# Kernel tuning notes

Hardware: AMD Instinct MI355X
Metric: run time of the kernel (lower is better)

Reference implementation:

```python
import jax, jax.numpy as jnp
import numpy as np

BATCH, SEQLEN, D_MODEL, D_STATE = 2, 2048, 512, 64
DT_MIN, DT_MAX = 1e-4, 1e-3


def setup_inputs() -> dict:
    key = jax.random.key(0)
    k1, k2, k3, k4 = jax.random.split(key, 4)
    u = jax.random.normal(k1, (BATCH, SEQLEN, D_MODEL), dtype=jnp.float32)
    # real parts of the complex params B, C (imag parts never affect the output)
    B_re = (jax.random.normal(k2, (D_STATE,), dtype=jnp.float32) / np.float32(np.sqrt(D_STATE)))
    C_re = (jax.random.normal(k3, (D_STATE,), dtype=jnp.float32) / np.float32(np.sqrt(D_STATE)))
    log_dt = jax.random.uniform(k4, (D_MODEL,), minval=np.log(DT_MIN), maxval=np.log(DT_MAX)).astype(jnp.float32)
    D = jnp.ones((D_MODEL,), dtype=jnp.float32)
    return {"u": u, "B_re": B_re, "C_re": C_re, "log_dt": log_dt, "D": D}


def reference(u, B_re, C_re, log_dt, D):
    # u: [B, L, H]; B_re/C_re: [N]; log_dt/D: [H]
    N = B_re.shape[0]
    # buffer: log_A = -0.5 * log(1 + n/N), n = 1..N  (A = exp(log_A) in (0,1])
    log_A = -0.5 * jnp.log1p(jnp.arange(1, N + 1, dtype=jnp.float32) / N)
    A = jnp.exp(log_A)                       # [N]
    delta = jnp.exp(log_dt)                  # [H]
    A_d = jnp.exp(delta[:, None] * A[None, :])          # [H, N]
    B_d = (A_d - 1.0) * B_re[None, :] * delta[:, None]  # [H, N]

    Bsz, L, H = u.shape
    x0 = jnp.zeros((Bsz, H, N), dtype=u.dtype)

    def step(x, u_t):                        # x: [B,H,N], u_t: [B,H]
        x = A_d * x + B_d * u_t[..., None]
        y_t = jnp.einsum('bhn,n->bh', x, C_re) + D * u_t
        return x, y_t

    _, ys = jax.lax.scan(step, x0, jnp.swapaxes(u, 0, 1))  # ys: [L,B,H]
    return jnp.swapaxes(ys, 0, 1)                          # [B,L,H]
```

## Files before the change

kernel.cpp:

```cpp
#include <hip/hip_runtime.h>
#include <math.h>


#define BATCH   2
#define SEQLEN  2048
#define DMODEL  512
#define DSTATE  64
#define T_CHUNK 32
#define NCHUNK  64

__device__ __forceinline__ float A_cont(int n) {
    return rsqrtf(1.0f + (float)(n + 1) * (1.0f / 64.0f));
}

__global__ __launch_bounds__(256) void k_tables(const float* __restrict__ B_re,
                                                const float* __restrict__ log_dt,
                                                float* __restrict__ AdT,
                                                float* __restrict__ BdT) {
    int tid = blockIdx.x * 256 + threadIdx.x;
    int h = tid & (DMODEL - 1);
    int n = tid >> 9;
    float delta = expf(log_dt[h]);
    float dA = delta * A_cont(n);
    AdT[n * DMODEL + h] = expf(dA);
    BdT[n * DMODEL + h] = expm1f(dA) * B_re[n] * delta;
}

__global__ __launch_bounds__(256) void k_xlocal(const float* __restrict__ u,
                                                const float* __restrict__ AdT,
                                                const float* __restrict__ BdT,
                                                float* __restrict__ xl) {
    int bid = (int)blockIdx.x;
    int wb  = (bid & 7) * 128 + (bid >> 3);
    int tid = wb * 256 + (int)threadIdx.x;
    int h  = tid & (DMODEL - 1);
    int ng = (tid >> 9) & 3;
    int c  = (tid >> 11) & (NCHUNK - 1);
    int b  = tid >> 17;
    int n0 = ng * 16;
    float Ad[16], Bd[16], x[16];
    #pragma unroll
    for (int nn = 0; nn < 16; ++nn) {
        Ad[nn] = AdT[(size_t)(n0 + nn) * DMODEL + h];
        Bd[nn] = BdT[(size_t)(n0 + nn) * DMODEL + h];
        x[nn] = 0.0f;
    }
    const float* up = u + ((size_t)(b * SEQLEN + c * T_CHUNK)) * DMODEL + h;
    #pragma unroll 8
    for (int s = 0; s < T_CHUNK; ++s) {
        float uv = up[(size_t)s * DMODEL];
        #pragma unroll
        for (int nn = 0; nn < 16; ++nn)
            x[nn] = fmaf(Ad[nn], x[nn], Bd[nn] * uv);
    }
    float* xp = xl + ((size_t)((b * NCHUNK + c) * DSTATE + n0)) * DMODEL + h;
    #pragma unroll
    for (int nn = 0; nn < 16; ++nn) xp[(size_t)nn * DMODEL] = x[nn];
}

__global__ __launch_bounds__(256) void k_scan(const float* __restrict__ log_dt,
                                              float* __restrict__ xl) {
    int tid = blockIdx.x * 256 + threadIdx.x;
    int h = tid & (DMODEL - 1);
    int n = (tid >> 9) & (DSTATE - 1);
    int b = tid >> 15;
    float delta = expf(log_dt[h]);
    float ApT = expf(delta * A_cont(n) * (float)T_CHUNK);
    float* base = xl + ((size_t)(b * NCHUNK * DSTATE + n)) * DMODEL + h;
    float v[NCHUNK - 1];
    #pragma unroll
    for (int c = 0; c < NCHUNK - 1; ++c)
        v[c] = base[(size_t)c * DSTATE * DMODEL];
    float s = 0.0f;
    #pragma unroll
    for (int c = 0; c < NCHUNK - 1; ++c) { s = fmaf(ApT, s, v[c]); v[c] = s; }
    #pragma unroll
    for (int c = 0; c < NCHUNK - 1; ++c)
        base[(size_t)c * DSTATE * DMODEL] = v[c];
}

__global__ __launch_bounds__(256) void k_y(const float* __restrict__ u,
                                           const float* __restrict__ AdT,
                                           const float* __restrict__ BdT,
                                           const float* __restrict__ C_re,
                                           const float* __restrict__ Dp,
                                           const float* __restrict__ Sbuf,
                                           float* __restrict__ out) {
    int bid = (int)blockIdx.x;
    int wb  = (bid & 7) * 128 + (bid >> 3);
    int tid = wb * 256 + (int)threadIdx.x;
    int hl = tid & 15;
    int ng = (tid >> 4) & 3;
    int hm = (tid >> 6) & 31;
    int h  = hl | (hm << 4);
    int c  = (tid >> 11) & (NCHUNK - 1);
    int b  = tid >> 17;
    int n0 = ng * 16;

    float Ad[16], Bd[16], Cw[16], x[16];
    #pragma unroll
    for (int nn = 0; nn < 16; ++nn) {
        Ad[nn] = AdT[(size_t)(n0 + nn) * DMODEL + h];
        Bd[nn] = BdT[(size_t)(n0 + nn) * DMODEL + h];
        Cw[nn] = C_re[n0 + nn];
    }
    if (c > 0) {
        const float* sp = Sbuf + ((size_t)((b * NCHUNK + (c - 1)) * DSTATE + n0)) * DMODEL + h;
        #pragma unroll
        for (int nn = 0; nn < 16; ++nn) x[nn] = sp[(size_t)nn * DMODEL];
    } else {
        #pragma unroll
        for (int nn = 0; nn < 16; ++nn) x[nn] = 0.0f;
    }
    float Dv = Dp[h];
    const float* up = u   + ((size_t)(b * SEQLEN + c * T_CHUNK)) * DMODEL + h;
    float*       op = out + ((size_t)(b * SEQLEN + c * T_CHUNK)) * DMODEL + h;
    int store_lane = ((threadIdx.x & 48) == 0);

    #pragma unroll 4
    for (int t = 0; t < T_CHUNK; ++t) {
        float uv = up[(size_t)t * DMODEL];
        #pragma unroll
        for (int nn = 0; nn < 16; ++nn)
            x[nn] = fmaf(Ad[nn], x[nn], Bd[nn] * uv);
        float a0 = 0.0f, a1 = 0.0f, a2 = 0.0f, a3 = 0.0f;
        #pragma unroll
        for (int nn = 0; nn < 16; nn += 4) {
            a0 = fmaf(Cw[nn + 0], x[nn + 0], a0);
            a1 = fmaf(Cw[nn + 1], x[nn + 1], a1);
            a2 = fmaf(Cw[nn + 2], x[nn + 2], a2);
            a3 = fmaf(Cw[nn + 3], x[nn + 3], a3);
        }
        float acc = (a0 + a1) + (a2 + a3);
        acc += __shfl_xor(acc, 16);
        acc += __shfl_xor(acc, 32);
        if (store_lane)
            __builtin_nontemporal_store(fmaf(Dv, uv, acc), &op[(size_t)t * DMODEL]);
    }
}

extern "C" void kernel_launch(void* const* d_in, const int* in_sizes, int n_in,
                              void* d_out, int out_size, void* d_ws, size_t ws_size,
                              hipStream_t stream) {
    const float* u      = (const float*)d_in[0];
    const float* B_re   = (const float*)d_in[1];
    const float* C_re   = (const float*)d_in[2];
    const float* log_dt = (const float*)d_in[3];
    const float* D      = (const float*)d_in[4];
    float* out = (float*)d_out;
    float* ws  = (float*)d_ws;

    float* AdT = ws;
    float* BdT = ws + 32768;
    float* xl  = ws + 65536;

    k_tables<<<128,  256, 0, stream>>>(B_re, log_dt, AdT, BdT);
    k_xlocal<<<1024, 256, 0, stream>>>(u, AdT, BdT, xl);
    k_scan  <<<256,  256, 0, stream>>>(log_dt, xl);
    k_y     <<<1024, 256, 0, stream>>>(u, AdT, BdT, C_re, D, xl, out);
}
```

Measured before the change: 110.1 us.

## Replace table and serial scan kernels with two-level in-block and in-kernel chunk scan

Removes the table kernel and the separate chunk-scan kernel, cutting four launches to two. k_ploc computes local chunk states, then combines groups of four micro-chunks through shared memory using powers of A_d. k_y rebuilds its starting state by summing the earlier macro-chunk results weighted by A_d powers. A_d and B_d are now computed inline with a cubic expm1 approximation, which relies on delta*A being small. Later chunks in k_y pay an extra loop of up to 15 macro terms, each reading 16 states per thread, and the A_d powers introduce some rounding differences.

```diff
diff --git a/kernel.cpp b/kernel.cpp
--- a/kernel.cpp
+++ b/kernel.cpp
@@ -6,119 +6,144 @@
 #define SEQLEN  2048
 #define DMODEL  512
 #define DSTATE  64
-#define T_CHUNK 32
-#define NCHUNK  64
+#define TMICRO  32
+#define NMICRO  64
+#define MPM     4
+#define NMACRO  16
 
 __device__ __forceinline__ float A_cont(int n) {
     return rsqrtf(1.0f + (float)(n + 1) * (1.0f / 64.0f));
 }
 
-__global__ __launch_bounds__(256) void k_tables(const float* __restrict__ B_re,
-                                                const float* __restrict__ log_dt,
-                                                float* __restrict__ AdT,
-                                                float* __restrict__ BdT) {
-    int tid = blockIdx.x * 256 + threadIdx.x;
-    int h = tid & (DMODEL - 1);
-    int n = tid >> 9;
-    float delta = expf(log_dt[h]);
-    float dA = delta * A_cont(n);
-    AdT[n * DMODEL + h] = expf(dA);
-    BdT[n * DMODEL + h] = expm1f(dA) * B_re[n] * delta;
+__device__ __forceinline__ float expm1_small(float x) {
+    return fmaf(fmaf(0.16666667f, x, 0.5f), x * x, x);
 }
 
-__global__ __launch_bounds__(256) void k_xlocal(const float* __restrict__ u,
-                                                const float* __restrict__ AdT,
-                                                const float* __restrict__ BdT,
-                                                float* __restrict__ xl) {
+__global__ __launch_bounds__(256) void k_ploc(const float* __restrict__ u,
+                                              const float* __restrict__ B_re,
+                                              const float* __restrict__ log_dt,
+                                              float* __restrict__ Ploc) {
+    __shared__ float sm[MPM][4][16][17];
     int bid = (int)blockIdx.x;
-    int wb  = (bid & 7) * 128 + (bid >> 3);
-    int tid = wb * 256 + (int)threadIdx.x;
-    int h  = tid & (DMODEL - 1);
-    int ng = (tid >> 9) & 3;
-    int c  = (tid >> 11) & (NCHUNK - 1);
-    int b  = tid >> 17;
+    int hh = bid & 7;
+    int k  = bid >> 3;
+    int b  = k >> 6;
+    int q2 = (k >> 4) & 3;
+    int mc = k & 15;
+    int tx = (int)threadIdx.x;
+    int hl = tx & 15;
+    int ng = (tx >> 4) & 3;
+    int cm = tx >> 6;
+    int h  = (hh << 6) | (q2 << 4) | hl;
+    int c  = mc * MPM + cm;
     int n0 = ng * 16;
-    float Ad[16], Bd[16], x[16];
+
+    float delta = expf(log_dt[h]);
+    float Ad[16], Bd[16], Ap[16], x[16];
     #pragma unroll
     for (int nn = 0; nn < 16; ++nn) {
-        Ad[nn] = AdT[(size_t)(n0 + nn) * DMODEL + h];
-        Bd[nn] = BdT[(size_t)(n0 + nn) * DMODEL + h];
+        int n = n0 + nn;
+        float dA = delta * A_cont(n);
+        float em = expm1_small(dA);
+        Ad[nn] = 1.0f + em;
+        Bd[nn] = em * B_re[n] * delta;
+        float p = Ad[nn];
+        p = p * p; p = p * p; p = p * p; p = p * p; p = p * p;
+        Ap[nn] = p;
         x[nn] = 0.0f;
     }
-    const float* up = u + ((size_t)(b * SEQLEN + c * T_CHUNK)) * DMODEL + h;
+    const float* up = u + ((size_t)(b * SEQLEN + c * TMICRO)) * DMODEL + h;
     #pragma unroll 8
-    for (int s = 0; s < T_CHUNK; ++s) {
+    for (int s = 0; s < TMICRO; ++s) {
         float uv = up[(size_t)s * DMODEL];
         #pragma unroll
         for (int nn = 0; nn < 16; ++nn)
             x[nn] = fmaf(Ad[nn], x[nn], Bd[nn] * uv);
     }
-    float* xp = xl + ((size_t)((b * NCHUNK + c) * DSTATE + n0)) * DMODEL + h;
     #pragma unroll
-    for (int nn = 0; nn < 16; ++nn) xp[(size_t)nn * DMODEL] = x[nn];
-}
-
-__global__ __launch_bounds__(256) void k_scan(const float* __restrict__ log_dt,
-                                              float* __restrict__ xl) {
-    int tid = blockIdx.x * 256 + threadIdx.x;
-    int h = tid & (DMODEL - 1);
-    int n = (tid >> 9) & (DSTATE - 1);
-    int b = tid >> 15;
-    float delta = expf(log_dt[h]);
-    float ApT = expf(delta * A_cont(n) * (float)T_CHUNK);
-    float* base = xl + ((size_t)(b * NCHUNK * DSTATE + n)) * DMODEL + h;
-    float v[NCHUNK - 1];
+    for (int nn = 0; nn < 16; ++nn) sm[cm][ng][nn][hl] = x[nn];
+    __syncthreads();
     #pragma unroll
-    for (int c = 0; c < NCHUNK - 1; ++c)
-        v[c] = base[(size_t)c * DSTATE * DMODEL];
-    float s = 0.0f;
+    for (int nn = 0; nn < 16; ++nn) {
+        float w = Ap[nn];
+        float p = x[nn];
+        for (int j = cm - 1; j >= 0; --j) {
+            p = fmaf(w, sm[j][ng][nn][hl], p);
+            w *= Ap[nn];
+        }
+        x[nn] = p;
+    }
+    float* pp = Ploc + ((size_t)((b * NMICRO + c) * DSTATE + n0)) * DMODEL + h;
     #pragma unroll
-    for (int c = 0; c < NCHUNK - 1; ++c) { s = fmaf(ApT, s, v[c]); v[c] = s; }
-    #pragma unroll
-    for (int c = 0; c < NCHUNK - 1; ++c)
-        base[(size_t)c * DSTATE * DMODEL] = v[c];
+    for (int nn = 0; nn < 16; ++nn) pp[(size_t)nn * DMODEL] = x[nn];
 }
 
 __global__ __launch_bounds__(256) void k_y(const float* __restrict__ u,
-                                           const float* __restrict__ AdT,
-                                           const float* __restrict__ BdT,
+                                           const float* __restrict__ B_re,
                                            const float* __restrict__ C_re,
+                                           const float* __restrict__ log_dt,
                                            const float* __restrict__ Dp,
-                                           const float* __restrict__ Sbuf,
+                                           const float* __restrict__ Ploc,
                                            float* __restrict__ out) {
     int bid = (int)blockIdx.x;
-    int wb  = (bid & 7) * 128 + (bid >> 3);
-    int tid = wb * 256 + (int)threadIdx.x;
-    int hl = tid & 15;
-    int ng = (tid >> 4) & 3;
-    int hm = (tid >> 6) & 31;
-    int h  = hl | (hm << 4);
-    int c  = (tid >> 11) & (NCHUNK - 1);
-    int b  = tid >> 17;
+    int hh = bid & 7;
+    int k  = bid >> 3;
+    int b  = k >> 6;
+    int c  = k & 63;
+    int tx = (int)threadIdx.x;
+    int hl = tx & 15;
+    int ng = (tx >> 4) & 3;
+    int hm2 = tx >> 6;
+    int h  = (hh << 6) | (hm2 << 4) | hl;
     int n0 = ng * 16;
+    int m = c >> 2, j = c & 3;
 
+    float delta = expf(log_dt[h]);
+    float Dv = Dp[h];
     float Ad[16], Bd[16], Cw[16], x[16];
     #pragma unroll
     for (int nn = 0; nn < 16; ++nn) {
-        Ad[nn] = AdT[(size_t)(n0 + nn) * DMODEL + h];
-        Bd[nn] = BdT[(size_t)(n0 + nn) * DMODEL + h];
-        Cw[nn] = C_re[n0 + nn];
+        int n = n0 + nn;
+        float dA = delta * A_cont(n);
+        float em = expm1_small(dA);
+        Ad[nn] = 1.0f + em;
+        Bd[nn] = em * B_re[n] * delta;
+        Cw[nn] = C_re[n];
+        x[nn] = 0.0f;
     }
-    if (c > 0) {
-        const float* sp = Sbuf + ((size_t)((b * NCHUNK + (c - 1)) * DSTATE + n0)) * DMODEL + h;
+    if (j > 0) {
+        const float* pp = Ploc + ((size_t)((b * NMICRO + (c - 1)) * DSTATE + n0)) * DMODEL + h;
         #pragma unroll
-        for (int nn = 0; nn < 16; ++nn) x[nn] = sp[(size_t)nn * DMODEL];
-    } else {
+        for (int nn = 0; nn < 16; ++nn) x[nn] = pp[(size_t)nn * DMODEL];
+    }
+    if (m > 0) {
+        float wj[16], w4[16];
         #pragma unroll
-        for (int nn = 0; nn < 16; ++nn) x[nn] = 0.0f;
+        for (int nn = 0; nn < 16; ++nn) {
+            float p = Ad[nn];
+            p = p * p; p = p * p; p = p * p; p = p * p; p = p * p;
+            float t2 = p * p;
+            float w = 1.0f;
+            if (j & 1) w = p;
+            if (j & 2) w *= t2;
+            wj[nn] = w;
+            w4[nn] = t2 * t2;
+        }
+        for (int mp = m - 1; mp >= 0; --mp) {
+            const float* ap = Ploc + ((size_t)((b * NMICRO + (mp * 4 + 3)) * DSTATE + n0)) * DMODEL + h;
+            #pragma unroll
+            for (int nn = 0; nn < 16; ++nn) {
+                x[nn] = fmaf(wj[nn], ap[(size_t)nn * DMODEL], x[nn]);
+                wj[nn] *= w4[nn];
+            }
+        }
     }
-    float Dv = Dp[h];
-    const float* up = u   + ((size_t)(b * SEQLEN + c * T_CHUNK)) * DMODEL + h;
-    float*       op = out + ((size_t)(b * SEQLEN + c * T_CHUNK)) * DMODEL + h;
-    int store_lane = ((threadIdx.x & 48) == 0);
+    const float* up = u   + ((size_t)(b * SEQLEN + c * TMICRO)) * DMODEL + h;
+    float*       op = out + ((size_t)(b * SEQLEN + c * TMICRO)) * DMODEL + h;
+    int store_lane = ((tx & 48) == 0);
 
     #pragma unroll 4
-    for (int t = 0; t < T_CHUNK; ++t) {
+    for (int t = 0; t < TMICRO; ++t) {
         float uv = up[(size_t)t * DMODEL];
         #pragma unroll
         for (int nn = 0; nn < 16; ++nn)
@@ -150,12 +175,8 @@
     float* out = (float*)d_out;
     float* ws  = (float*)d_ws;
 
-    float* AdT = ws;
-    float* BdT = ws + 32768;
-    float* xl  = ws + 65536;
+    float* Ploc = ws;
 
-    k_tables<<<128,  256, 0, stream>>>(B_re, log_dt, AdT, BdT);
-    k_xlocal<<<1024, 256, 0, stream>>>(u, AdT, BdT, xl);
-    k_scan  <<<256,  256, 0, stream>>>(log_dt, xl);
-    k_y     <<<1024, 256, 0, stream>>>(u, AdT, BdT, C_re, D, xl, out);
+    k_ploc<<<1024, 256, 0, stream>>>(u, B_re, log_dt, Ploc);
+    k_y   <<<1024, 256, 0, stream>>>(u, B_re, C_re, log_dt, D, Ploc, out);
 }
```

Result: faster. 106.9 us (-2.9%).
